# Performance work log

Hardware: AMD Instinct MI355X
Metric: run time of the kernel (lower is better)

## Reference

```python
import jax, jax.numpy as jnp
import numpy as np
from jax import lax

KS = 3
N = KS * KS


def _conv(x, W, b, pad, stride):
    out = lax.conv_general_dilated(
        x, W, window_strides=(stride, stride),
        padding=[(pad, pad), (pad, pad)],
        dimension_numbers=("NCHW", "OIHW", "NCHW"))
    return out + b[None, :, None, None]


def setup_inputs() -> dict:
    key = jax.random.key(0)
    ks = jax.random.split(key, 5)
    b, c, h, w, outc = 16, 64, 64, 64, 128
    return {
        "x": jax.random.normal(ks[0], (b, c, h, w), jnp.float32),
        "W_off": jax.random.normal(ks[1], (2 * N, c, KS, KS), jnp.float32) * 0.05,
        "b_off": jax.random.normal(ks[2], (2 * N,), jnp.float32) * 0.05,
        "W_k": jax.random.normal(ks[3], (outc, c, KS, KS), jnp.float32) * 0.05,
        "b_k": jax.random.normal(ks[4], (outc,), jnp.float32) * 0.05,
    }


def _deform_conv(x, W_off, b_off, W_k, b_k):
    b, c, h, w = x.shape
    offset = _conv(x, W_off, b_off, pad=1, stride=1)  # [b, 2N, h, w]

    # kernel-grid offsets, flattened with x (row) index first: n = i*ks + j
    rng = jnp.arange(KS, dtype=x.dtype) - (KS - 1) // 2  # [-1, 0, 1]
    pnx = jnp.repeat(rng, KS)  # [N]
    pny = jnp.tile(rng, KS)    # [N]

    # sampling positions p = p0 + p_n + offset, clamped into the image
    px = jnp.arange(h, dtype=x.dtype)[None, None, :, None] + pnx[None, :, None, None] + offset[:, :N]
    py = jnp.arange(w, dtype=x.dtype)[None, None, None, :] + pny[None, :, None, None] + offset[:, N:]
    px = jnp.clip(px, 0, h - 1)
    py = jnp.clip(py, 0, w - 1)

    fx = jnp.floor(px)
    fy = jnp.floor(py)
    tx = px - fx  # fractional parts (bilinear weights)
    ty = py - fy
    x0 = fx.astype(jnp.int32)
    y0 = fy.astype(jnp.int32)
    x1 = jnp.minimum(x0 + 1, h - 1)  # out-of-range tap carries zero weight
    y1 = jnp.minimum(y0 + 1, w - 1)

    x_hw = x.transpose(0, 2, 3, 1).reshape(b, h * w, c)  # [b, hw, c]

    def gather(ix, iy):
        idx = (ix * w + iy).reshape(b, -1, 1)  # [b, N*h*w, 1]
        return jnp.take_along_axis(x_hw, idx, axis=1).reshape(b, N, h, w, c)

    wx0, wx1 = (1 - tx)[..., None], tx[..., None]
    wy0, wy1 = (1 - ty)[..., None], ty[..., None]
    # 4-tap bilinear interpolation == the original's sparse G @ x
    xo = (gather(x0, y0) * wx0 * wy0 + gather(x1, y0) * wx1 * wy0
          + gather(x0, y1) * wx0 * wy1 + gather(x1, y1) * wx1 * wy1)  # [b,N,h,w,c]

    # _reshape_x_offset: out[b,c, i_h*ks+i, i_w*ks+j] = xo[b, i*ks+j, i_h, i_w, c]
    xo = xo.reshape(b, KS, KS, h, w, c).transpose(0, 5, 3, 1, 4, 2)
    xo = xo.reshape(b, c, h * KS, w * KS)

    return _conv(xo, W_k, b_k, pad=0, stride=KS)  # [b, outc, h, w]


def reference(x, W_off, b_off, W_k, b_k):
    return _deform_conv(x, W_off, b_off, W_k, b_k)
```

## Files before the change

kernel.cpp:

```cpp
#include <hip/hip_runtime.h>

typedef __attribute__((ext_vector_type(8))) short bf16x8;
typedef __attribute__((ext_vector_type(4))) float floatx4;

__device__ __forceinline__ unsigned short f2bf(float f) {
    unsigned int u = __float_as_uint(f);
    u += 0x7FFFu + ((u >> 16) & 1u);
    return (unsigned short)(u >> 16);
}

__global__ __launch_bounds__(256) void prep_all(const float* __restrict__ x,
        const float* __restrict__ Wk, const float* __restrict__ Woff,
        unsigned short* __restrict__ xt, unsigned short* __restrict__ Wkb2,
        unsigned short* __restrict__ Woffb) {
    int bb = blockIdx.x;
    if (bb < 1024) {
        __shared__ float tile[64][65];
        int b = bb >> 6, y = bb & 63;
        const float* src = x + (size_t)b * 262144 + y * 64;
        int tx = threadIdx.x & 15, tg = threadIdx.x >> 4;
#pragma unroll
        for (int i = 0; i < 4; i++) {
            int c = tg + i * 16;
            float4 v = *(const float4*)(src + (size_t)c * 4096 + tx * 4);
            tile[c][tx * 4 + 0] = v.x; tile[c][tx * 4 + 1] = v.y;
            tile[c][tx * 4 + 2] = v.z; tile[c][tx * 4 + 3] = v.w;
        }
        __syncthreads();
        unsigned short* dst = xt + (size_t)bb * 4096;
#pragma unroll
        for (int i = 0; i < 4; i++) {
            int xc = tg + i * 16;
            int c4 = tx * 4;
            ushort4 v;
            v.x = f2bf(tile[c4 + 0][xc]); v.y = f2bf(tile[c4 + 1][xc]);
            v.z = f2bf(tile[c4 + 2][xc]); v.w = f2bf(tile[c4 + 3][xc]);
            *(ushort4*)(dst + xc * 64 + c4) = v;
        }
    } else if (bb < 1312) {
        int idx = (bb - 1024) * 256 + threadIdx.x;
        int tap = idx >> 13;
        int r = idx & 8191;
        int tile = r >> 9;
        int ln = (r >> 3) & 63;
        int j = r & 7;
        int mt = tile >> 1, kc = tile & 1;
        int oc = mt * 16 + (ln & 15);
        int c = kc * 32 + (ln >> 4) * 8 + j;
        Wkb2[idx] = f2bf(Wk[(oc * 64 + c) * 9 + tap]);
    } else {
        int idx = (bb - 1312) * 256 + threadIdx.x;
        int tap = idx >> 11;
        int r = idx & 2047;
        int tile = r >> 9;
        int ln = (r >> 3) & 63;
        int j = r & 7;
        int mt = tile >> 1, kc = tile & 1;
        int n = mt * 16 + (ln & 15);
        int c = kc * 32 + (ln >> 4) * 8 + j;
        float v = (n < 18) ? Woff[(n * 64 + c) * 9 + tap] : 0.f;
        Woffb[idx] = f2bf(v);
    }
}

__global__ __launch_bounds__(256, 4) void fused_kernel(
        const unsigned short* __restrict__ xt,
        const unsigned short* __restrict__ Wkb2,
        const unsigned short* __restrict__ Woffb,
        const float* __restrict__ boff,
        const float* __restrict__ bias,
        float* __restrict__ out) {
    __shared__ unsigned short As[2][8192];
    __shared__ float offs[64][20];
    int tid = threadIdx.x;
    int wave = tid >> 6, lane = tid & 63;
    int frow = lane & 15, quad = lane >> 4;
    int bb = blockIdx.x;
    int xcd = bb & 7, idx = bb >> 3;
    int b = xcd * 2 + (idx >> 6);
    int pxBase = (idx & 63) * 64;
    int pl = wave * 16 + frow;
    int px = pxBase + pl;
    int y = px >> 6, xx = px & 63;
    const char* img = (const char*)(xt + (size_t)b * 262144) + quad * 16;

    float bv[2][4];
#pragma unroll
    for (int mt = 0; mt < 2; mt++)
#pragma unroll
        for (int rg = 0; rg < 4; rg++) {
            int n = mt * 16 + quad * 4 + rg;
            bv[mt][rg] = (n < 18) ? boff[n] : 0.f;
        }

    floatx4 acc1[2];
    acc1[0] = (floatx4)(0.f); acc1[1] = (floatx4)(0.f);
    bf16x8 aw = *(const bf16x8*)(Woffb + tid * 8);
    *(bf16x8*)&As[0][tid * 8] = aw;
    for (int tap = 0; tap < 9; tap++) {
        if (tap < 8) aw = *(const bf16x8*)(Woffb + (tap + 1) * 2048 + tid * 8);
        __syncthreads();
        int ry = y + tap / 3 - 1, rx = xx + tap % 3 - 1;
        bool valid = (ry >= 0) & (ry < 64) & (rx >= 0) & (rx < 64);
        const char* src = img + ((ry * 64 + rx) << 7);
        const unsigned short* abuf = &As[tap & 1][0];
        bf16x8 bz = {};
#pragma unroll
        for (int kc = 0; kc < 2; kc++) {
            bf16x8 bfr = valid ? *(const bf16x8*)(src + kc * 64) : bz;
#pragma unroll
            for (int mt = 0; mt < 2; mt++) {
                bf16x8 af = *(const bf16x8*)&abuf[(mt * 2 + kc) * 512 + lane * 8];
                acc1[mt] = __builtin_amdgcn_mfma_f32_16x16x32_bf16(af, bfr, acc1[mt], 0, 0, 0);
            }
        }
        if (tap < 8) *(bf16x8*)&As[(tap + 1) & 1][tid * 8] = aw;
    }
#pragma unroll
    for (int mt = 0; mt < 2; mt++)
#pragma unroll
        for (int rg = 0; rg < 4; rg++) {
            int n = mt * 16 + quad * 4 + rg;
            if (n < 18) offs[pl][n] = acc1[mt][rg] + bv[mt][rg];
        }

    floatx4 acc[8];
#pragma unroll
    for (int i = 0; i < 8; i++) acc[i] = (floatx4)(0.f);
    bf16x8 wk[4];
#pragma unroll
    for (int i = 0; i < 4; i++)
        wk[i] = *(const bf16x8*)(Wkb2 + i * 2048 + tid * 8);
    __syncthreads();
#pragma unroll
    for (int i = 0; i < 4; i++)
        *(bf16x8*)&As[0][i * 2048 + tid * 8] = wk[i];

    for (int tap = 0; tap < 9; tap++) {
        if (tap < 8)
#pragma unroll
            for (int i = 0; i < 4; i++)
                wk[i] = *(const bf16x8*)(Wkb2 + (tap + 1) * 8192 + i * 2048 + tid * 8);
        __syncthreads();
        float orow = offs[pl][tap];
        float ocol = offs[pl][9 + tap];
        float pr = (float)(y + tap / 3 - 1) + orow;
        float pc = (float)(xx + tap % 3 - 1) + ocol;
        pr = fminf(fmaxf(pr, 0.f), 63.f);
        pc = fminf(fmaxf(pc, 0.f), 63.f);
        float fr = floorf(pr), fc = floorf(pc);
        float tr = pr - fr, tc = pc - fc;
        int r0 = (int)fr, c0 = (int)fc;
        int r1 = min(r0 + 1, 63), c1 = min(c0 + 1, 63);
        float w00 = (1.f - tr) * (1.f - tc);
        float w01 = (1.f - tr) * tc;
        float w10 = tr * (1.f - tc);
        float w11 = tr * tc;
        int o00 = (r0 * 64 + c0) * 128;
        int o01 = (r0 * 64 + c1) * 128;
        int o10 = (r1 * 64 + c0) * 128;
        int o11 = (r1 * 64 + c1) * 128;

        bf16x8 bfrag[2];
#pragma unroll
        for (int kc = 0; kc < 2; kc++) {
            int4 u00 = __builtin_bit_cast(int4, *(const bf16x8*)(img + o00 + kc * 64));
            int4 u01 = __builtin_bit_cast(int4, *(const bf16x8*)(img + o01 + kc * 64));
            int4 u10 = __builtin_bit_cast(int4, *(const bf16x8*)(img + o10 + kc * 64));
            int4 u11 = __builtin_bit_cast(int4, *(const bf16x8*)(img + o11 + kc * 64));
            int4 r;
#pragma unroll
            for (int wd = 0; wd < 4; wd++) {
                int a00 = (wd == 0) ? u00.x : (wd == 1) ? u00.y : (wd == 2) ? u00.z : u00.w;
                int a01 = (wd == 0) ? u01.x : (wd == 1) ? u01.y : (wd == 2) ? u01.z : u01.w;
                int a10 = (wd == 0) ? u10.x : (wd == 1) ? u10.y : (wd == 2) ? u10.z : u10.w;
                int a11 = (wd == 0) ? u11.x : (wd == 1) ? u11.y : (wd == 2) ? u11.z : u11.w;
                float vl = w00 * __uint_as_float((unsigned)a00 << 16)
                         + w01 * __uint_as_float((unsigned)a01 << 16)
                         + w10 * __uint_as_float((unsigned)a10 << 16)
                         + w11 * __uint_as_float((unsigned)a11 << 16);
                float vh = w00 * __uint_as_float((unsigned)a00 & 0xffff0000u)
                         + w01 * __uint_as_float((unsigned)a01 & 0xffff0000u)
                         + w10 * __uint_as_float((unsigned)a10 & 0xffff0000u)
                         + w11 * __uint_as_float((unsigned)a11 & 0xffff0000u);
                unsigned pk = __builtin_amdgcn_perm(
                    __float_as_uint(vh) + 0x8000u,
                    __float_as_uint(vl) + 0x8000u, 0x07060302u);
                if (wd == 0) r.x = (int)pk; else if (wd == 1) r.y = (int)pk;
                else if (wd == 2) r.z = (int)pk; else r.w = (int)pk;
            }
            bfrag[kc] = __builtin_bit_cast(bf16x8, r);
        }
        const unsigned short* abuf = &As[tap & 1][0];
#pragma unroll
        for (int kc = 0; kc < 2; kc++)
#pragma unroll
            for (int mt = 0; mt < 8; mt++) {
                bf16x8 af = *(const bf16x8*)&abuf[(mt * 2 + kc) * 512 + lane * 8];
                acc[mt] = __builtin_amdgcn_mfma_f32_16x16x32_bf16(af, bfrag[kc], acc[mt], 0, 0, 0);
            }
        if (tap < 8)
#pragma unroll
            for (int i = 0; i < 4; i++)
                *(bf16x8*)&As[(tap + 1) & 1][i * 2048 + tid * 8] = wk[i];
    }

    float* outb = out + (size_t)b * 524288 + px;
#pragma unroll
    for (int mt = 0; mt < 8; mt++) {
#pragma unroll
        for (int rg = 0; rg < 4; rg++) {
            int oc = mt * 16 + quad * 4 + rg;
            outb[oc * 4096] = acc[mt][rg] + bias[oc];
        }
    }
}

extern "C" void kernel_launch(void* const* d_in, const int* in_sizes, int n_in,
                              void* d_out, int out_size, void* d_ws, size_t ws_size,
                              hipStream_t stream) {
    const float* x    = (const float*)d_in[0];
    const float* Woff = (const float*)d_in[1];
    const float* boff = (const float*)d_in[2];
    const float* Wk   = (const float*)d_in[3];
    const float* bk   = (const float*)d_in[4];
    float* out = (float*)d_out;

    char* ws = (char*)d_ws;
    unsigned short* xt    = (unsigned short*)ws;
    unsigned short* Wkb2  = (unsigned short*)(ws + 8388608);
    unsigned short* Woffb = (unsigned short*)(ws + 8536064);

    prep_all<<<1384, 256, 0, stream>>>(x, Wk, Woff, xt, Wkb2, Woffb);
    fused_kernel<<<1024, 256, 0, stream>>>(xt, Wkb2, Woffb, boff, bk, out);
}
```

Baseline: 132.3 us.

## Load MFMA weight fragments directly from global memory instead of LDS staging

Removes the double-buffered LDS staging of offset-conv and main-conv weight fragments. Each wave now reads its A-fragments directly from global memory (L1/L2 cached) per tap, which eliminates the per-tap __syncthreads barriers and the LDS stores. A single barrier remains after the offsets are written. The trade is that every wave fetches the weights redundantly from cache, with global-load latency on the MFMA critical path. In exchange, LDS usage drops and the block-wide sync overhead goes away.

```diff
diff --git a/kernel.cpp b/kernel.cpp
--- a/kernel.cpp
+++ b/kernel.cpp
@@ -70,7 +70,6 @@
         const float* __restrict__ boff,
         const float* __restrict__ bias,
         float* __restrict__ out) {
-    __shared__ unsigned short As[2][8192];
     __shared__ float offs[64][20];
     int tid = threadIdx.x;
     int wave = tid >> 6, lane = tid & 63;
@@ -83,65 +82,41 @@
     int px = pxBase + pl;
     int y = px >> 6, xx = px & 63;
     const char* img = (const char*)(xt + (size_t)b * 262144) + quad * 16;
-
-    float bv[2][4];
-#pragma unroll
-    for (int mt = 0; mt < 2; mt++)
-#pragma unroll
-        for (int rg = 0; rg < 4; rg++) {
-            int n = mt * 16 + quad * 4 + rg;
-            bv[mt][rg] = (n < 18) ? boff[n] : 0.f;
-        }
+    const unsigned short* wofL = Woffb + lane * 8;
+    const unsigned short* wkL  = Wkb2 + lane * 8;
 
     floatx4 acc1[2];
     acc1[0] = (floatx4)(0.f); acc1[1] = (floatx4)(0.f);
-    bf16x8 aw = *(const bf16x8*)(Woffb + tid * 8);
-    *(bf16x8*)&As[0][tid * 8] = aw;
     for (int tap = 0; tap < 9; tap++) {
-        if (tap < 8) aw = *(const bf16x8*)(Woffb + (tap + 1) * 2048 + tid * 8);
-        __syncthreads();
         int ry = y + tap / 3 - 1, rx = xx + tap % 3 - 1;
         bool valid = (ry >= 0) & (ry < 64) & (rx >= 0) & (rx < 64);
         const char* src = img + ((ry * 64 + rx) << 7);
-        const unsigned short* abuf = &As[tap & 1][0];
         bf16x8 bz = {};
+        const unsigned short* wt = wofL + tap * 2048;
 #pragma unroll
         for (int kc = 0; kc < 2; kc++) {
             bf16x8 bfr = valid ? *(const bf16x8*)(src + kc * 64) : bz;
 #pragma unroll
             for (int mt = 0; mt < 2; mt++) {
-                bf16x8 af = *(const bf16x8*)&abuf[(mt * 2 + kc) * 512 + lane * 8];
+                bf16x8 af = *(const bf16x8*)(wt + (mt * 2 + kc) * 512);
                 acc1[mt] = __builtin_amdgcn_mfma_f32_16x16x32_bf16(af, bfr, acc1[mt], 0, 0, 0);
             }
         }
-        if (tap < 8) *(bf16x8*)&As[(tap + 1) & 1][tid * 8] = aw;
     }
 #pragma unroll
     for (int mt = 0; mt < 2; mt++)
 #pragma unroll
         for (int rg = 0; rg < 4; rg++) {
             int n = mt * 16 + quad * 4 + rg;
-            if (n < 18) offs[pl][n] = acc1[mt][rg] + bv[mt][rg];
-        }
+            if (n < 18) offs[pl][n] = acc1[mt][rg] + boff[n];
+        }
+    __syncthreads();
 
     floatx4 acc[8];
 #pragma unroll
     for (int i = 0; i < 8; i++) acc[i] = (floatx4)(0.f);
-    bf16x8 wk[4];
-#pragma unroll
-    for (int i = 0; i < 4; i++)
-        wk[i] = *(const bf16x8*)(Wkb2 + i * 2048 + tid * 8);
-    __syncthreads();
-#pragma unroll
-    for (int i = 0; i < 4; i++)
-        *(bf16x8*)&As[0][i * 2048 + tid * 8] = wk[i];
 
     for (int tap = 0; tap < 9; tap++) {
-        if (tap < 8)
-#pragma unroll
-            for (int i = 0; i < 4; i++)
-                wk[i] = *(const bf16x8*)(Wkb2 + (tap + 1) * 8192 + i * 2048 + tid * 8);
-        __syncthreads();
         float orow = offs[pl][tap];
         float ocol = offs[pl][9 + tap];
         float pr = (float)(y + tap / 3 - 1) + orow;
@@ -160,8 +135,8 @@
         int o01 = (r0 * 64 + c1) * 128;
         int o10 = (r1 * 64 + c0) * 128;
         int o11 = (r1 * 64 + c1) * 128;
-
-        bf16x8 bfrag[2];
+        const unsigned short* wt = wkL + tap * 8192;
+
 #pragma unroll
         for (int kc = 0; kc < 2; kc++) {
             int4 u00 = __builtin_bit_cast(int4, *(const bf16x8*)(img + o00 + kc * 64));
@@ -189,20 +164,13 @@
                 if (wd == 0) r.x = (int)pk; else if (wd == 1) r.y = (int)pk;
                 else if (wd == 2) r.z = (int)pk; else r.w = (int)pk;
             }
-            bfrag[kc] = __builtin_bit_cast(bf16x8, r);
-        }
-        const unsigned short* abuf = &As[tap & 1][0];
-#pragma unroll
-        for (int kc = 0; kc < 2; kc++)
+            bf16x8 bfrag = __builtin_bit_cast(bf16x8, r);
 #pragma unroll
             for (int mt = 0; mt < 8; mt++) {
-                bf16x8 af = *(const bf16x8*)&abuf[(mt * 2 + kc) * 512 + lane * 8];
-                acc[mt] = __builtin_amdgcn_mfma_f32_16x16x32_bf16(af, bfrag[kc], acc[mt], 0, 0, 0);
+                bf16x8 af = *(const bf16x8*)(wt + (mt * 2 + kc) * 512);
+                acc[mt] = __builtin_amdgcn_mfma_f32_16x16x32_bf16(af, bfrag, acc[mt], 0, 0, 0);
             }
-        if (tap < 8)
-#pragma unroll
-            for (int i = 0; i < 4; i++)
-                *(bf16x8*)&As[(tap + 1) & 1][i * 2048 + tid * 8] = wk[i];
+        }
     }
 
     float* outb = out + (size_t)b * 524288 + px;
```

New measurement: 144.4 us. 1.09x slower.
